# Optimization experiments

Hardware: AMD Instinct MI355X
Metric: run time of the kernel (lower is better)

Reference implementation:

```python
import jax, jax.numpy as jnp
import numpy as np

N_GRID = 5
ORDER = 3
X_MIN = -1.0
X_MAX = 1.0
N_BASIS = N_GRID + ORDER - 1  # 7
EPS = 1e-8


def _make_grid():
    # order repeated endpoints on each side of n_grid interior knots
    interior = jnp.linspace(X_MIN, X_MAX, N_GRID, dtype=jnp.float32)
    left = jnp.full((ORDER,), X_MIN, dtype=jnp.float32)
    right = jnp.full((ORDER,), X_MAX, dtype=jnp.float32)
    return jnp.concatenate([left, interior, right])  # (n_grid + 2*order,) = (11,)


def _b_spline_basis(xc, grid):
    """Vectorized Cox-de Boor over all input dims at once.
    xc: (N, d_in) clamped to [X_MIN, X_MAX]. Returns (N, d_in, N_BASIS)."""
    xe = xc[..., None]  # (N, d_in, 1)
    # degree-0 indicator basis on each knot interval
    basis = ((xe >= grid[:-1]) & (xe < grid[1:])).astype(xc.dtype)
    # right-closed last interval: x == grid[-1] counts for last basis
    basis = basis.at[..., -1].add((xc == grid[-1]).astype(xc.dtype))
    for k in range(1, ORDER + 1):
        n_k = grid.shape[0] - k - 1
        denom_l = jnp.maximum(grid[k:n_k + k] - grid[:n_k], EPS)
        coeff_l = (xe - grid[:n_k]) / denom_l
        denom_r = jnp.maximum(grid[k + 1:n_k + k + 1] - grid[1:n_k + 1], EPS)
        coeff_r = (grid[k + 1:n_k + k + 1] - xe) / denom_r
        basis = coeff_l * basis[..., :n_k] + coeff_r * basis[..., 1:n_k + 1]
    return basis  # (N, d_in, N_BASIS)


def setup_inputs() -> dict:
    key = jax.random.key(0)
    k1, k2, k3 = jax.random.split(key, 3)
    N, d_in, d_out = 8192, 1024, 1024
    x = jax.random.normal(k1, (N, d_in), dtype=jnp.float32)
    # coeff is zero-init in torch; use small random values so spline path is exercised
    coeff = jax.random.normal(k2, (d_out, d_in, N_BASIS), dtype=jnp.float32) * 0.1
    w_base = jax.random.normal(k3, (d_out, d_in), dtype=jnp.float32) * (1.0 / np.sqrt(d_in))
    bias = jnp.zeros((d_out,), dtype=jnp.float32)
    return {"x": x, "coeff": coeff, "w_base": w_base, "bias": bias}


def reference(x, coeff, w_base, bias):
    grid = _make_grid()
    xc = jnp.clip(x, X_MIN, X_MAX)               # (N, d_in)
    basis = _b_spline_basis(xc, grid)            # (N, d_in, n_basis)
    y_spline = jnp.einsum('nib,oib->no', basis, coeff)  # (N, d_out)
    y_base = jax.nn.silu(xc) @ w_base.T          # (N, d_out)
    return y_spline + y_base + bias
```

## Files before the change

kernel.cpp:

```cpp
#include <hip/hip_runtime.h>

#define D_IN   1024
#define D_OUT  1024
#define KB_CNT (D_IN / 8)
#define IMG_BYTES 16384
#define COL_TILES (D_OUT / 128)

typedef __attribute__((ext_vector_type(8))) short bf16x8;
typedef __attribute__((ext_vector_type(4))) float f32x4;
typedef __attribute__((ext_vector_type(4))) unsigned int u32x4;

typedef __attribute__((address_space(1))) unsigned int as1_u32;
typedef __attribute__((address_space(3))) unsigned int as3_u32;

__device__ __forceinline__ void gload_lds16(const void* g, void* l) {
  __builtin_amdgcn_global_load_lds((const as1_u32*)(unsigned long long)g,
                                   (as3_u32*)(unsigned int)(unsigned long long)l,
                                   16, 0, 0);
}

__device__ __forceinline__ unsigned short f2bf(float f) {
  unsigned int u = __float_as_uint(f);
  u += 0x7fffu + ((u >> 16) & 1u);
  return (unsigned short)(u >> 16);
}

__device__ __forceinline__ float basis_and_silu(float xv, float* b) {
  float xc = fminf(fmaxf(xv, -1.f), 1.f);
  const float G[11] = {-1.f, -1.f, -1.f, -1.f, -0.5f, 0.f, 0.5f, 1.f, 1.f, 1.f, 1.f};
  float t[10];
#pragma unroll
  for (int j = 0; j < 10; j++)
    t[j] = (xc >= G[j] && xc < G[j + 1]) ? 1.f : 0.f;
  t[9] += (xc == 1.f) ? 1.f : 0.f;
#pragma unroll
  for (int k = 1; k <= 3; k++) {
#pragma unroll
    for (int j = 0; j < 10 - k; j++) {
      float dl = G[j + k] - G[j];
      float il = 1.f / (dl < 1e-8f ? 1e-8f : dl);
      float dr = G[j + k + 1] - G[j + 1];
      float ir = 1.f / (dr < 1e-8f ? 1e-8f : dr);
      t[j] = (xc - G[j]) * il * t[j] + (G[j + k + 1] - xc) * ir * t[j + 1];
    }
  }
#pragma unroll
  for (int j = 0; j < 7; j++) b[j] = t[j];
  return xc / (1.f + __expf(-xc));
}

__global__ __launch_bounds__(256) void prep_kernel(const float* __restrict__ coeff,
                                                   const float* __restrict__ w_base,
                                                   char* __restrict__ bp) {
  int tid = blockIdx.x * 256 + threadIdx.x;
  int o = tid >> 10;
  int i = tid & (D_IN - 1);

  float v[8];
#pragma unroll
  for (int b = 0; b < 7; b++) v[b] = coeff[(size_t)tid * 7 + b];
  v[7] = w_base[tid];

  union { unsigned short h[8]; u32x4 q; } u;
#pragma unroll
  for (int b = 0; b < 8; b++) u.h[b] = f2bf(v[b]);

  int tileC = o >> 7, cl = o & 127, kb = i >> 3, il = i & 7;
  size_t img = ((size_t)(tileC * KB_CNT + kb)) * IMG_BYTES;
  int off = (cl * 128 + il * 16) ^ ((cl & 7) << 4);
  *(u32x4*)(bp + img + off) = u.q;
}

__global__ __launch_bounds__(256) void act_kernel(const float* __restrict__ x,
                                                  char* __restrict__ ap) {
  int tid = blockIdx.x * 256 + threadIdx.x;
  int row = tid >> 8;
  int iq = (tid & 255) * 4;

  float4 xv = *(const float4*)(x + ((size_t)row << 10) + iq);
  float xs[4] = {xv.x, xv.y, xv.z, xv.w};

  int tile = row >> 7, r = row & 127;
  int roff = r * 128;
  int xorm = (r & 7) << 4;

#pragma unroll
  for (int e = 0; e < 4; e++) {
    float b[7];
    float s = basis_and_silu(xs[e], b);
    union { unsigned short h[8]; u32x4 q; } u;
#pragma unroll
    for (int q2 = 0; q2 < 7; q2++) u.h[q2] = f2bf(b[q2]);
    u.h[7] = f2bf(s);
    int i = iq + e;
    int kb = i >> 3, il = i & 7;
    size_t img = ((size_t)(tile * KB_CNT + kb)) * IMG_BYTES;
    int off = (roff + il * 16) ^ xorm;
    *(u32x4*)(ap + img + off) = u.q;
  }
}

#define BUFB 49152

__global__ __launch_bounds__(512, 2) void gemm8_kernel(const char* __restrict__ ap,
                                                       const char* __restrict__ bp,
                                                       const float* __restrict__ bias,
                                                       float* __restrict__ out) {
  __shared__ __align__(16) char lds[3 * BUFB];

  const int nwg = gridDim.x;
  const int orig = blockIdx.x;
  const int q = nwg >> 3, r = nwg & 7;
  const int xcd = orig & 7, seq = orig >> 3;
  const int wg = (xcd < r ? xcd * (q + 1) : r * (q + 1) + (xcd - r) * q) + seq;
  const int tileR = wg >> 3;
  const int tileC = wg & 7;

  const int tid = threadIdx.x;
  const int lane = tid & 63;
  const int w = tid >> 6;
  const int wm = w >> 1, wn = w & 1;

  const char* pa0 = ap + ((size_t)(tileR * 2 + 0) * KB_CNT) * IMG_BYTES + tid * 16;
  const char* pa1 = ap + ((size_t)(tileR * 2 + 1) * KB_CNT) * IMG_BYTES + tid * 16;
  const char* pb  = bp + ((size_t)tileC * KB_CNT) * IMG_BYTES + tid * 16;
  char* lw = lds + w * 1024;

  f32x4 acc[4][4];
#pragma unroll
  for (int m = 0; m < 4; m++)
#pragma unroll
    for (int n = 0; n < 4; n++) acc[m][n] = (f32x4){0.f, 0.f, 0.f, 0.f};

  const int xm = (lane & 7) << 4;
  const int arow = wm * 64 + (lane & 15);
  const int bcol = wn * 64 + (lane & 15);
  const int kch = (lane >> 4) * 16;

#pragma unroll
  for (int ss = 0; ss < 2; ++ss) {
    gload_lds16(pa0,        lw + ss * BUFB);
    gload_lds16(pa0 + 8192, lw + ss * BUFB + 8192);
    gload_lds16(pa1,        lw + ss * BUFB + 16384);
    gload_lds16(pa1 + 8192, lw + ss * BUFB + 24576);
    gload_lds16(pb,         lw + ss * BUFB + 32768);
    gload_lds16(pb + 8192,  lw + ss * BUFB + 40960);
    pa0 += IMG_BYTES; pa1 += IMG_BYTES; pb += IMG_BYTES;
  }
  asm volatile("s_waitcnt vmcnt(6)" ::: "memory");
  __builtin_amdgcn_s_barrier();

  int bsel = 0, ssel = 2;
  for (int t = 0; t < KB_CNT; ++t) {
    const char* lb = lds + bsel * BUFB;
    char* sw = lw + ssel * BUFB;
    const bool stg = (t + 2) < KB_CNT;
    bf16x8 af[2][2], bfr[4][2], ag[2][2];

#pragma unroll
    for (int c = 0; c < 2; ++c) {
      af[c][0] = *(const bf16x8*)(lb + (((arow + c * 16) * 128 + kch) ^ xm));
      af[c][1] = *(const bf16x8*)(lb + (((arow + c * 16) * 128 + 64 + kch) ^ xm));
    }
#pragma unroll
    for (int n = 0; n < 4; ++n) {
      bfr[n][0] = *(const bf16x8*)(lb + 32768 + (((bcol + n * 16) * 128 + kch) ^ xm));
      bfr[n][1] = *(const bf16x8*)(lb + 32768 + (((bcol + n * 16) * 128 + 64 + kch) ^ xm));
    }
    if (stg) {
      gload_lds16(pa0,        sw);
      gload_lds16(pa0 + 8192, sw + 8192);
      gload_lds16(pa1,        sw + 16384);
    }
    __builtin_amdgcn_s_barrier();
    asm volatile("s_waitcnt lgkmcnt(0)" ::: "memory");
    __builtin_amdgcn_s_setprio(1);
#pragma unroll
    for (int c = 0; c < 2; ++c)
#pragma unroll
      for (int n = 0; n < 4; ++n) {
        acc[c][n] = __builtin_amdgcn_mfma_f32_16x16x32_bf16(af[c][0], bfr[n][0], acc[c][n], 0, 0, 0);
        acc[c][n] = __builtin_amdgcn_mfma_f32_16x16x32_bf16(af[c][1], bfr[n][1], acc[c][n], 0, 0, 0);
      }
    __builtin_amdgcn_s_setprio(0);
    __builtin_amdgcn_s_barrier();

#pragma unroll
    for (int c = 0; c < 2; ++c) {
      ag[c][0] = *(const bf16x8*)(lb + (((arow + (c + 2) * 16) * 128 + kch) ^ xm));
      ag[c][1] = *(const bf16x8*)(lb + (((arow + (c + 2) * 16) * 128 + 64 + kch) ^ xm));
    }
    if (stg) {
      gload_lds16(pa1 + 8192, sw + 24576);
      gload_lds16(pb,         sw + 32768);
      gload_lds16(pb + 8192,  sw + 40960);
    }
    if (t < KB_CNT - 2) { asm volatile("s_waitcnt vmcnt(6)" ::: "memory"); }
    else                { asm volatile("s_waitcnt vmcnt(0)" ::: "memory"); }
    __builtin_amdgcn_s_barrier();
    asm volatile("s_waitcnt lgkmcnt(0)" ::: "memory");
    __builtin_amdgcn_s_setprio(1);
#pragma unroll
    for (int c = 0; c < 2; ++c)
#pragma unroll
      for (int n = 0; n < 4; ++n) {
        acc[c + 2][n] = __builtin_amdgcn_mfma_f32_16x16x32_bf16(ag[c][0], bfr[n][0], acc[c + 2][n], 0, 0, 0);
        acc[c + 2][n] = __builtin_amdgcn_mfma_f32_16x16x32_bf16(ag[c][1], bfr[n][1], acc[c + 2][n], 0, 0, 0);
      }
    __builtin_amdgcn_s_setprio(0);
    __builtin_amdgcn_s_barrier();

    if (stg) { pa0 += IMG_BYTES; pa1 += IMG_BYTES; pb += IMG_BYTES; }
    bsel = bsel == 2 ? 0 : bsel + 1;
    ssel = ssel == 2 ? 0 : ssel + 1;
  }

  const int r0 = tileR * 256 + wm * 64 + ((lane >> 4) * 4);
  const int c0 = tileC * 128 + wn * 64 + (lane & 15);
#pragma unroll
  for (int m = 0; m < 4; m++) {
#pragma unroll
    for (int n = 0; n < 4; n++) {
      int c = c0 + n * 16;
      float bv = bias[c];
#pragma unroll
      for (int j = 0; j < 4; j++) {
        int rr = r0 + m * 16 + j;
        out[(size_t)rr * D_OUT + c] = acc[m][n][j] + bv;
      }
    }
  }
}

__global__ __launch_bounds__(256) void naive_kernel(const float* __restrict__ x,
                                                    const float* __restrict__ coeff,
                                                    const float* __restrict__ w_base,
                                                    const float* __restrict__ bias,
                                                    float* __restrict__ out) {
  __shared__ float sb[D_IN][8];
  const int n = blockIdx.x >> 2;
  const int o = (blockIdx.x & 3) * 256 + threadIdx.x;

  for (int i = threadIdx.x; i < D_IN; i += 256) {
    float b[7];
    float s = basis_and_silu(x[(size_t)n * D_IN + i], b);
#pragma unroll
    for (int qd = 0; qd < 7; qd++) sb[i][qd] = b[qd];
    sb[i][7] = s;
  }
  __syncthreads();

  float acc = bias[o];
  for (int i = 0; i < D_IN; i++) {
    const float* cp = coeff + ((size_t)o * D_IN + i) * 7;
    float p = sb[i][7] * w_base[(size_t)o * D_IN + i];
#pragma unroll
    for (int qd = 0; qd < 7; qd++) p += sb[i][qd] * cp[qd];
    acc += p;
  }
  out[(size_t)n * D_OUT + o] = acc;
}

extern "C" void kernel_launch(void* const* d_in, const int* in_sizes, int n_in,
                              void* d_out, int out_size, void* d_ws, size_t ws_size,
                              hipStream_t stream) {
  const float* x      = (const float*)d_in[0];
  const float* coeff  = (const float*)d_in[1];
  const float* w_base = (const float*)d_in[2];
  const float* bias   = (const float*)d_in[3];
  float* out = (float*)d_out;

  const int n_rows = in_sizes[0] / D_IN;
  const int row_tiles = n_rows / 128;

  const size_t bp_bytes = (size_t)COL_TILES * KB_CNT * IMG_BYTES;
  const size_t tile_bytes = (size_t)KB_CNT * IMG_BYTES;

  if (ws_size < bp_bytes + 2 * tile_bytes) {
    naive_kernel<<<n_rows * 4, 256, 0, stream>>>(x, coeff, w_base, bias, out);
    return;
  }

  char* bpw = (char*)d_ws;
  char* apb = bpw + bp_bytes;
  size_t avail = ws_size - bp_bytes;
  int chunk_tiles = (int)(avail / tile_bytes) & ~1;
  if (chunk_tiles > row_tiles) chunk_tiles = row_tiles;

  prep_kernel<<<(D_OUT * D_IN) / 256, 256, 0, stream>>>(coeff, w_base, bpw);

  for (int t0 = 0; t0 < row_tiles; t0 += chunk_tiles) {
    int nt = (row_tiles - t0 < chunk_tiles) ? (row_tiles - t0) : chunk_tiles;
    act_kernel<<<nt * 128, 256, 0, stream>>>(x + (size_t)t0 * 128 * D_IN, apb);
    gemm8_kernel<<<(nt / 2) * COL_TILES, 512, 0, stream>>>(
        apb, bpw, bias, out + (size_t)t0 * 128 * D_OUT);
  }
}
```

Measured before the change: 277.6 us.

## Load B fragments directly into registers and coalesce activation packing through LDS

The GEMM no longer stages the weight (B) tile through LDS. Each wave reads its B fragments straight from global memory into registers, double-buffered across an unrolled-by-two K loop, which shrinks each LDS stage from 48KB to 32KB. Separately, the activation-packing kernel first stages an 8x128 block of x in shared memory, then has threads write contiguous swizzled image slots, so its global stores are better coalesced. The cost is that B global-load latency is only partly hidden: the vmcnt wait also drains the next B loads. Several waves now re-read the same B data from cache instead of sharing it through LDS.

```diff
diff --git a/kernel.cpp b/kernel.cpp
--- a/kernel.cpp
+++ b/kernel.cpp
@@ -5,6 +5,7 @@
 #define KB_CNT (D_IN / 8)
 #define IMG_BYTES 16384
 #define COL_TILES (D_OUT / 128)
+#define BUFB 32768
 
 typedef __attribute__((ext_vector_type(8))) short bf16x8;
 typedef __attribute__((ext_vector_type(4))) float f32x4;
@@ -73,34 +74,42 @@
 
 __global__ __launch_bounds__(256) void act_kernel(const float* __restrict__ x,
                                                   char* __restrict__ ap) {
-  int tid = blockIdx.x * 256 + threadIdx.x;
-  int row = tid >> 8;
-  int iq = (tid & 255) * 4;
-
-  float4 xv = *(const float4*)(x + ((size_t)row << 10) + iq);
-  float xs[4] = {xv.x, xv.y, xv.z, xv.w};
-
-  int tile = row >> 7, r = row & 127;
-  int roff = r * 128;
-  int xorm = (r & 7) << 4;
+  __shared__ float xs[8][136];
+
+  const int rg = blockIdx.x >> 3;
+  const int kg = blockIdx.x & 7;
+  const int t = threadIdx.x;
+
+#pragma unroll
+  for (int rep = 0; rep < 4; rep++) {
+    int idx = rep * 256 + t;
+    int r = idx >> 7, ii = idx & 127;
+    xs[r][ii] = x[((size_t)(rg * 8 + r) << 10) + kg * 128 + ii];
+  }
+  __syncthreads();
+
+  const int il = t & 7;
+  const int rl = (t >> 3) & 7;
+  const int wv = t >> 6;
+  const int tile = rg >> 4;
+  const int r = (rg & 15) * 8 + rl;
+  const int off = (r * 128 + il * 16) ^ (rl << 4);
 
 #pragma unroll
   for (int e = 0; e < 4; e++) {
+    int kb_loc = wv * 4 + e;
+    float xvv = xs[rl][kb_loc * 8 + il];
     float b[7];
-    float s = basis_and_silu(xs[e], b);
+    float s = basis_and_silu(xvv, b);
     union { unsigned short h[8]; u32x4 q; } u;
 #pragma unroll
     for (int q2 = 0; q2 < 7; q2++) u.h[q2] = f2bf(b[q2]);
     u.h[7] = f2bf(s);
-    int i = iq + e;
-    int kb = i >> 3, il = i & 7;
+    int kb = kg * 16 + kb_loc;
     size_t img = ((size_t)(tile * KB_CNT + kb)) * IMG_BYTES;
-    int off = (roff + il * 16) ^ xorm;
     *(u32x4*)(ap + img + off) = u.q;
   }
 }
-
-#define BUFB 49152
 
 __global__ __launch_bounds__(512, 2) void gemm8_kernel(const char* __restrict__ ap,
                                                        const char* __restrict__ bp,
@@ -110,9 +119,9 @@
 
   const int nwg = gridDim.x;
   const int orig = blockIdx.x;
-  const int q = nwg >> 3, r = nwg & 7;
+  const int q = nwg >> 3, rq = nwg & 7;
   const int xcd = orig & 7, seq = orig >> 3;
-  const int wg = (xcd < r ? xcd * (q + 1) : r * (q + 1) + (xcd - r) * q) + seq;
+  const int wg = (xcd < rq ? xcd * (q + 1) : rq * (q + 1) + (xcd - rq) * q) + seq;
   const int tileR = wg >> 3;
   const int tileC = wg & 7;
 
@@ -123,7 +132,7 @@
 
   const char* pa0 = ap + ((size_t)(tileR * 2 + 0) * KB_CNT) * IMG_BYTES + tid * 16;
   const char* pa1 = ap + ((size_t)(tileR * 2 + 1) * KB_CNT) * IMG_BYTES + tid * 16;
-  const char* pb  = bp + ((size_t)tileC * KB_CNT) * IMG_BYTES + tid * 16;
+  const char* pbi = bp + ((size_t)tileC * KB_CNT) * IMG_BYTES;
   char* lw = lds + w * 1024;
 
   f32x4 acc[4][4];
@@ -137,83 +146,96 @@
   const int bcol = wn * 64 + (lane & 15);
   const int kch = (lane >> 4) * 16;
 
-#pragma unroll
-  for (int ss = 0; ss < 2; ++ss) {
-    gload_lds16(pa0,        lw + ss * BUFB);
-    gload_lds16(pa0 + 8192, lw + ss * BUFB + 8192);
-    gload_lds16(pa1,        lw + ss * BUFB + 16384);
-    gload_lds16(pa1 + 8192, lw + ss * BUFB + 24576);
-    gload_lds16(pb,         lw + ss * BUFB + 32768);
-    gload_lds16(pb + 8192,  lw + ss * BUFB + 40960);
-    pa0 += IMG_BYTES; pa1 += IMG_BYTES; pb += IMG_BYTES;
-  }
-  asm volatile("s_waitcnt vmcnt(6)" ::: "memory");
+  bf16x8 Bc[4][2], Bn[4][2];
+
+  gload_lds16(pa0,        lw);
+  gload_lds16(pa0 + 8192, lw + 8192);
+  gload_lds16(pa1,        lw + 16384);
+  gload_lds16(pa1 + 8192, lw + 24576);
+  pa0 += IMG_BYTES; pa1 += IMG_BYTES;
+#pragma unroll
+  for (int n = 0; n < 4; ++n) {
+    Bc[n][0] = *(const bf16x8*)(pbi + (((bcol + n * 16) * 128 + kch) ^ xm));
+    Bc[n][1] = *(const bf16x8*)(pbi + (((bcol + n * 16) * 128 + 64 + kch) ^ xm));
+  }
+  gload_lds16(pa0,        lw + BUFB);
+  gload_lds16(pa0 + 8192, lw + BUFB + 8192);
+  gload_lds16(pa1,        lw + BUFB + 16384);
+  gload_lds16(pa1 + 8192, lw + BUFB + 24576);
+  pa0 += IMG_BYTES; pa1 += IMG_BYTES;
+  const char* pbn = pbi + IMG_BYTES;
+  asm volatile("s_waitcnt vmcnt(4)" ::: "memory");
   __builtin_amdgcn_s_barrier();
 
-  int bsel = 0, ssel = 2;
-  for (int t = 0; t < KB_CNT; ++t) {
-    const char* lb = lds + bsel * BUFB;
-    char* sw = lw + ssel * BUFB;
-    const bool stg = (t + 2) < KB_CNT;
-    bf16x8 af[2][2], bfr[4][2], ag[2][2];
-
-#pragma unroll
-    for (int c = 0; c < 2; ++c) {
-      af[c][0] = *(const bf16x8*)(lb + (((arow + c * 16) * 128 + kch) ^ xm));
-      af[c][1] = *(const bf16x8*)(lb + (((arow + c * 16) * 128 + 64 + kch) ^ xm));
-    }
-#pragma unroll
-    for (int n = 0; n < 4; ++n) {
-      bfr[n][0] = *(const bf16x8*)(lb + 32768 + (((bcol + n * 16) * 128 + kch) ^ xm));
-      bfr[n][1] = *(const bf16x8*)(lb + 32768 + (((bcol + n * 16) * 128 + 64 + kch) ^ xm));
-    }
-    if (stg) {
-      gload_lds16(pa0,        sw);
-      gload_lds16(pa0 + 8192, sw + 8192);
-      gload_lds16(pa1,        sw + 16384);
-    }
-    __builtin_amdgcn_s_barrier();
-    asm volatile("s_waitcnt lgkmcnt(0)" ::: "memory");
-    __builtin_amdgcn_s_setprio(1);
-#pragma unroll
-    for (int c = 0; c < 2; ++c)
-#pragma unroll
-      for (int n = 0; n < 4; ++n) {
-        acc[c][n] = __builtin_amdgcn_mfma_f32_16x16x32_bf16(af[c][0], bfr[n][0], acc[c][n], 0, 0, 0);
-        acc[c][n] = __builtin_amdgcn_mfma_f32_16x16x32_bf16(af[c][1], bfr[n][1], acc[c][n], 0, 0, 0);
-      }
-    __builtin_amdgcn_s_setprio(0);
-    __builtin_amdgcn_s_barrier();
-
-#pragma unroll
-    for (int c = 0; c < 2; ++c) {
-      ag[c][0] = *(const bf16x8*)(lb + (((arow + (c + 2) * 16) * 128 + kch) ^ xm));
-      ag[c][1] = *(const bf16x8*)(lb + (((arow + (c + 2) * 16) * 128 + 64 + kch) ^ xm));
-    }
-    if (stg) {
-      gload_lds16(pa1 + 8192, sw + 24576);
-      gload_lds16(pb,         sw + 32768);
-      gload_lds16(pb + 8192,  sw + 40960);
-    }
-    if (t < KB_CNT - 2) { asm volatile("s_waitcnt vmcnt(6)" ::: "memory"); }
-    else                { asm volatile("s_waitcnt vmcnt(0)" ::: "memory"); }
-    __builtin_amdgcn_s_barrier();
-    asm volatile("s_waitcnt lgkmcnt(0)" ::: "memory");
-    __builtin_amdgcn_s_setprio(1);
-#pragma unroll
-    for (int c = 0; c < 2; ++c)
-#pragma unroll
-      for (int n = 0; n < 4; ++n) {
-        acc[c + 2][n] = __builtin_amdgcn_mfma_f32_16x16x32_bf16(ag[c][0], bfr[n][0], acc[c + 2][n], 0, 0, 0);
-        acc[c + 2][n] = __builtin_amdgcn_mfma_f32_16x16x32_bf16(ag[c][1], bfr[n][1], acc[c + 2][n], 0, 0, 0);
-      }
-    __builtin_amdgcn_s_setprio(0);
-    __builtin_amdgcn_s_barrier();
-
-    if (stg) { pa0 += IMG_BYTES; pa1 += IMG_BYTES; pb += IMG_BYTES; }
-    bsel = bsel == 2 ? 0 : bsel + 1;
-    ssel = ssel == 2 ? 0 : ssel + 1;
-  }
+#define TILE_BODY(T, BCUR, BNXT, LB, SW)                                        \
+  {                                                                             \
+    const char* lb = (LB);                                                      \
+    bf16x8 a0[2][2];                                                            \
+    _Pragma("unroll")                                                           \
+    for (int c = 0; c < 2; ++c) {                                               \
+      a0[c][0] = *(const bf16x8*)(lb + (((arow + c * 16) * 128 + kch) ^ xm));   \
+      a0[c][1] = *(const bf16x8*)(lb + (((arow + c * 16) * 128 + 64 + kch) ^ xm)); \
+    }                                                                           \
+    if ((T) + 1 < KB_CNT) {                                                     \
+      _Pragma("unroll")                                                         \
+      for (int n = 0; n < 4; ++n) {                                             \
+        BNXT[n][0] = *(const bf16x8*)(pbn + (((bcol + n * 16) * 128 + kch) ^ xm)); \
+        BNXT[n][1] = *(const bf16x8*)(pbn + (((bcol + n * 16) * 128 + 64 + kch) ^ xm)); \
+      }                                                                         \
+    }                                                                           \
+    if ((T) + 2 < KB_CNT) {                                                     \
+      gload_lds16(pa0,        (SW));                                            \
+      gload_lds16(pa0 + 8192, (SW) + 8192);                                     \
+    }                                                                           \
+    __builtin_amdgcn_s_barrier();                                               \
+    asm volatile("s_waitcnt lgkmcnt(0)" ::: "memory");                          \
+    __builtin_amdgcn_s_setprio(1);                                              \
+    _Pragma("unroll")                                                           \
+    for (int c = 0; c < 2; ++c)                                                 \
+      _Pragma("unroll")                                                         \
+      for (int n = 0; n < 4; ++n) {                                             \
+        acc[c][n] = __builtin_amdgcn_mfma_f32_16x16x32_bf16(a0[c][0], BCUR[n][0], acc[c][n], 0, 0, 0); \
+        acc[c][n] = __builtin_amdgcn_mfma_f32_16x16x32_bf16(a0[c][1], BCUR[n][1], acc[c][n], 0, 0, 0); \
+      }                                                                         \
+    __builtin_amdgcn_s_setprio(0);                                              \
+    __builtin_amdgcn_s_barrier();                                               \
+    _Pragma("unroll")                                                           \
+    for (int c = 0; c < 2; ++c) {                                               \
+      a0[c][0] = *(const bf16x8*)(lb + (((arow + (c + 2) * 16) * 128 + kch) ^ xm)); \
+      a0[c][1] = *(const bf16x8*)(lb + (((arow + (c + 2) * 16) * 128 + 64 + kch) ^ xm)); \
+    }                                                                           \
+    if ((T) + 2 < KB_CNT) {                                                     \
+      gload_lds16(pa1,        (SW) + 16384);                                    \
+      gload_lds16(pa1 + 8192, (SW) + 24576);                                    \
+      pa0 += IMG_BYTES; pa1 += IMG_BYTES;                                       \
+    }                                                                           \
+    pbn += IMG_BYTES;                                                           \
+    if ((T) < KB_CNT - 2) { asm volatile("s_waitcnt vmcnt(4)" ::: "memory"); }  \
+    else                  { asm volatile("s_waitcnt vmcnt(0)" ::: "memory"); }  \
+    __builtin_amdgcn_s_barrier();                                               \
+    asm volatile("s_waitcnt lgkmcnt(0)" ::: "memory");                          \
+    __builtin_amdgcn_s_setprio(1);                                              \
+    _Pragma("unroll")                                                           \
+    for (int c = 0; c < 2; ++c)                                                 \
+      _Pragma("unroll")                                                         \
+      for (int n = 0; n < 4; ++n) {                                             \
+        acc[c + 2][n] = __builtin_amdgcn_mfma_f32_16x16x32_bf16(a0[c][0], BCUR[n][0], acc[c + 2][n], 0, 0, 0); \
+        acc[c + 2][n] = __builtin_amdgcn_mfma_f32_16x16x32_bf16(a0[c][1], BCUR[n][1], acc[c + 2][n], 0, 0, 0); \
+      }                                                                         \
+    __builtin_amdgcn_s_setprio(0);                                              \
+    __builtin_amdgcn_s_barrier();                                               \
+  }
+
+  int bsel = 0;
+  for (int t = 0; t < KB_CNT; t += 2) {
+    const int s0 = bsel + 2 > 2 ? bsel - 1 : bsel + 2;
+    TILE_BODY(t, Bc, Bn, lds + bsel * BUFB, lw + s0 * BUFB);
+    const int b1 = bsel + 1 > 2 ? 0 : bsel + 1;
+    const int s1 = b1 + 2 > 2 ? b1 - 1 : b1 + 2;
+    TILE_BODY(t + 1, Bn, Bc, lds + b1 * BUFB, lw + s1 * BUFB);
+    bsel = b1 + 1 > 2 ? 0 : b1 + 1;
+  }
+#undef TILE_BODY
 
   const int r0 = tileR * 256 + wm * 64 + ((lane >> 4) * 4);
   const int c0 = tileC * 128 + wn * 64 + (lane & 15);
@@ -291,7 +313,7 @@
 
   for (int t0 = 0; t0 < row_tiles; t0 += chunk_tiles) {
     int nt = (row_tiles - t0 < chunk_tiles) ? (row_tiles - t0) : chunk_tiles;
-    act_kernel<<<nt * 128, 256, 0, stream>>>(x + (size_t)t0 * 128 * D_IN, apb);
+    act_kernel<<<nt * 16 * 8, 256, 0, stream>>>(x + (size_t)t0 * 128 * D_IN, apb);
     gemm8_kernel<<<(nt / 2) * COL_TILES, 512, 0, stream>>>(
         apb, bpw, bias, out + (size_t)t0 * 128 * D_OUT);
   }
```

New measurement: 320.4 us. 15.4% more time.
